# Kernel optimization log

Hardware: AMD Instinct MI355X
Metric: run time of the kernel (lower is better)

Reference implementation:

```python
import jax, jax.numpy as jnp
import numpy as np

N_NODES = 50000
D_IN = 256
D_OUT = 128
N_POS = 1600000   # positive edges used for GCN aggregation
N_PRED = 500000   # edges to score


def setup_inputs() -> dict:
    key = jax.random.key(0)
    ks = jax.random.split(key, 6)
    x = jax.random.normal(ks[0], (N_NODES, D_IN), dtype=jnp.float32)
    pos_edge_index = jax.random.randint(ks[1], (2, N_POS), 0, N_NODES)
    edge_index = jax.random.randint(ks[2], (2, N_PRED), 0, N_NODES)
    # init_linear: Linear(d_in, d_in); stored as (in, out) so fwd is x @ W1 + b1
    W1 = jax.random.normal(ks[3], (D_IN, D_IN), dtype=jnp.float32) / np.sqrt(D_IN).astype(np.float32)
    b1 = jnp.zeros((D_IN,), dtype=jnp.float32)
    # GCNConv weight (in, out) and bias
    Wc = jax.random.normal(ks[4], (D_IN, D_OUT), dtype=jnp.float32) / np.sqrt(D_IN).astype(np.float32)
    bc = jnp.zeros((D_OUT,), dtype=jnp.float32)
    return dict(x=x, edge_index=edge_index, pos_edge_index=pos_edge_index,
                W1=W1, b1=b1, Wc=Wc, bc=bc)


def reference(x, edge_index, pos_edge_index, W1, b1, Wc, bc):
    n = x.shape[0]
    # init_linear
    h = x @ W1 + b1                                  # [N, D_IN]
    # GCNConv: linear transform first, then normalized scatter-add aggregation
    h = h @ Wc                                       # [N, D_OUT]
    # add self-loops (PyG GCNConv default add_self_loops=True, edge_weight=1)
    loops = jnp.arange(n, dtype=pos_edge_index.dtype)
    row = jnp.concatenate([pos_edge_index[0], loops])  # source
    col = jnp.concatenate([pos_edge_index[1], loops])  # target (aggregation)
    # symmetric normalization: deg over target, norm = d^-1/2[row]*d^-1/2[col]
    deg = jax.ops.segment_sum(jnp.ones_like(col, dtype=h.dtype), col, num_segments=n)
    dinv = jnp.where(deg > 0, jax.lax.rsqrt(deg), 0.0)
    norm = dinv[row] * dinv[col]                     # [E+N]
    msgs = h[row] * norm[:, None]                    # gather + scale
    out = jax.ops.segment_sum(msgs, col, num_segments=n) + bc  # scatter-add + bias
    # edge dot-product scoring
    logits = (out[edge_index[0]] * out[edge_index[1]]).sum(axis=-1)  # [N_PRED]
    return logits
```

## Files before the change

kernel.cpp:

```cpp
#include <hip/hip_runtime.h>

#define N_NODES 50000
#define D_IN 256
#define D_OUT 128
#define N_POS 1600000
#define N_PRED 500000

#define G_BUCKETS 782
#define GPAD 1024
#define SB 640
#define CHUNK 2500
#define CAP 4096
#define GEMM_BLOCKS 782
#define QPRED 125000

#define NT 4
#define TSZ 12500
#define NPB 32
#define AGGB 1563

typedef __attribute__((ext_vector_type(8))) short short8;
typedef __attribute__((ext_vector_type(4))) float f32x4;

__device__ __forceinline__ unsigned short f2bf(float f) {
    unsigned int u = __float_as_uint(f);
    u += 0x7FFFu + ((u >> 16) & 1u);
    return (unsigned short)(u >> 16);
}
__device__ __forceinline__ unsigned int pk2(float a, float b) {
    unsigned int ua = __float_as_uint(a), ub = __float_as_uint(b);
    ua += 0x7FFFu + ((ua >> 16) & 1u);
    ub += 0x7FFFu + ((ub >> 16) & 1u);
    return (ua >> 16) | (ub & 0xFFFF0000u);
}
__device__ __forceinline__ float bflo(unsigned int u) { return __uint_as_float(u << 16); }
__device__ __forceinline__ float bfhi(unsigned int u) { return __uint_as_float(u & 0xFFFF0000u); }

__device__ __forceinline__ float dot8(uint4 ua, uint4 ub) {
    return bflo(ua.x) * bflo(ub.x) + bfhi(ua.x) * bfhi(ub.x)
         + bflo(ua.y) * bflo(ub.y) + bfhi(ua.y) * bfhi(ub.y)
         + bflo(ua.z) * bflo(ub.z) + bfhi(ua.z) * bfhi(ub.z)
         + bflo(ua.w) * bflo(ub.w) + bfhi(ua.w) * bfhi(ub.w);
}

__global__ void fuse_weights_k(const float* __restrict__ W1, const float* __restrict__ Wc,
                               const float* __restrict__ b1,
                               unsigned short* __restrict__ Bp, float* __restrict__ bf) {
    int gid = blockIdx.x * blockDim.x + threadIdx.x;
    int k = gid >> 7;
    int n = gid & 127;
    float acc = 0.f;
    #pragma unroll 4
    for (int kk = 0; kk < D_IN; ++kk)
        acc += W1[k * D_IN + kk] * Wc[kk * D_OUT + n];
    int ks = k >> 5, q = (k >> 3) & 3, jj = k & 7;
    int nt = n >> 4, nl = n & 15;
    int lane = q * 16 + nl;
    Bp[(((long)(ks * 8 + nt)) * 64 + lane) * 8 + jj] = f2bf(acc);
    if (gid < D_OUT) {
        float accb = 0.f;
        for (int kk = 0; kk < D_IN; ++kk)
            accb += b1[kk] * Wc[kk * D_OUT + gid];
        bf[gid] = accb;
    }
}

__global__ __launch_bounds__(256) void scatter_gemm_k(const int* __restrict__ row,
                                                      const int* __restrict__ col,
                                                      unsigned int* __restrict__ seg,
                                                      unsigned int* __restrict__ ebs,
                                                      const float* __restrict__ x,
                                                      const uint4* __restrict__ Bp,
                                                      const float* __restrict__ bf,
                                                      unsigned short* __restrict__ hsb) {
    __shared__ __align__(16) char smem[23424];
    if (blockIdx.x < SB) {
        int* hist  = (int*)smem;
        int* lofs  = hist + GPAD;
        int* fill2 = lofs + GPAD;
        int* part  = fill2 + GPAD;
        unsigned int* stag = (unsigned int*)(part + 256);
        int t = threadIdx.x;
        int b = blockIdx.x;
        for (int i = t; i < GPAD; i += 256) { hist[i] = 0; fill2[i] = 0; }
        __syncthreads();
        int e0 = b * CHUNK;
        for (int i = t; i < CHUNK; i += 256)
            atomicAdd(&hist[col[e0 + i] >> 6], 1);
        __syncthreads();
        int h[4], p4 = 0;
        #pragma unroll
        for (int i = 0; i < 4; ++i) { h[i] = hist[4 * t + i]; p4 += h[i]; }
        part[t] = p4;
        __syncthreads();
        for (int d = 1; d < 256; d <<= 1) {
            int add = (t >= d) ? part[t - d] : 0;
            __syncthreads();
            part[t] += add;
            __syncthreads();
        }
        int ex = part[t] - p4;
        #pragma unroll
        for (int i = 0; i < 4; ++i) { lofs[4 * t + i] = ex; ex += h[i]; }
        __syncthreads();
        for (int g = t; g < G_BUCKETS; g += 256)
            seg[(long)g * SB + b] = (unsigned int)lofs[g] | ((unsigned int)hist[g] << 16);
        for (int i = t; i < CHUNK; i += 256) {
            int c = col[e0 + i];
            int g = c >> 6;
            unsigned int u = (unsigned int)row[e0 + i] | ((unsigned int)(c & 63) << 16);
            int lp = atomicAdd(&fill2[g], 1);
            stag[lofs[g] + lp] = u;
        }
        __syncthreads();
        for (int i = t; i < CHUNK; i += 256)
            ebs[(long)b * CHUNK + i] = stag[i];
    } else {
        const int gb   = blockIdx.x - SB;
        const int wave = threadIdx.x >> 6;
        const int lane = threadIdx.x & 63;
        const int q    = lane >> 4;
        const int ml   = lane & 15;
        const int m0   = gb * 64 + wave * 16;

        f32x4 acc[8];
        #pragma unroll
        for (int t = 0; t < 8; ++t) acc[t] = (f32x4){0.f, 0.f, 0.f, 0.f};

        long arow = m0 + ml; if (arow > N_NODES - 1) arow = N_NODES - 1;
        const float* xrow = x + arow * D_IN + q * 8;

        #pragma unroll
        for (int ks = 0; ks < 8; ++ks) {
            float4 xa = *(const float4*)(xrow + ks * 32);
            float4 xb = *(const float4*)(xrow + ks * 32 + 4);
            union { short8 s; unsigned int u[4]; } af;
            af.u[0] = pk2(xa.x, xa.y);
            af.u[1] = pk2(xa.z, xa.w);
            af.u[2] = pk2(xb.x, xb.y);
            af.u[3] = pk2(xb.z, xb.w);
            #pragma unroll
            for (int nt = 0; nt < 8; ++nt) {
                union { uint4 v; short8 s; } bu;
                bu.v = Bp[(long)(ks * 8 + nt) * 64 + lane];
                acc[nt] = __builtin_amdgcn_mfma_f32_16x16x32_bf16(af.s, bu.s, acc[nt], 0, 0, 0);
            }
        }

        unsigned short* o = (unsigned short*)smem + wave * 2048;
        #pragma unroll
        for (int nt = 0; nt < 8; ++nt) {
            float bn = bf[nt * 16 + ml];
            #pragma unroll
            for (int r = 0; r < 4; ++r) {
                float val = acc[nt][r] + bn;
                o[(q * 4 + r) * 128 + nt * 16 + ml] = f2bf(val);
            }
        }
        __syncthreads();
        #pragma unroll
        for (int i = 0; i < 4; ++i) {
            int fb = i * 1024 + lane * 16;
            int v = m0 + (fb >> 8);
            if (v < N_NODES) {
                uint4 val = *(const uint4*)((const char*)o + fb);
                *(uint4*)((char*)hsb + (long)v * 256 + (fb & 255)) = val;
            }
        }
    }
}

__global__ __launch_bounds__(256) void csr_build_k(const unsigned int* __restrict__ seg,
                                                   const unsigned int* __restrict__ ebs,
                                                   unsigned short* __restrict__ csr,
                                                   int* __restrict__ offs5,
                                                   float* __restrict__ dinv,
                                                   uint4* __restrict__ hsb4) {
    __shared__ unsigned int stag[CAP];
    __shared__ unsigned short stag2[CAP];
    __shared__ int hist[256], lofs[256], fill[256], part[256];
    __shared__ float dloc[64];
    __shared__ int scnt;
    int t = threadIdx.x;
    int g = blockIdx.x;
    int s = g * CAP;
    hist[t] = 0; fill[t] = 0;
    const unsigned int* sg = seg + (long)g * SB;
    unsigned int w0 = sg[t];
    unsigned int w1 = sg[t + 256];
    unsigned int w2 = (t + 512 < SB) ? sg[t + 512] : 0u;
    int c0 = w0 >> 16, c1 = w1 >> 16, c2 = w2 >> 16;
    int lsum = c0 + c1 + c2;
    part[t] = lsum;
    __syncthreads();
    for (int d = 1; d < 256; d <<= 1) {
        int add = (t >= d) ? part[t - d] : 0;
        __syncthreads();
        part[t] += add;
        __syncthreads();
    }
    if (t == 255) scnt = part[255];
    int p = part[t] - lsum;
    {
        const unsigned int* e0p = ebs + (long)t * CHUNK + (w0 & 0xFFFFu);
        for (int k = 0; k < c0; ++k) stag[p + k] = e0p[k];
        p += c0;
        const unsigned int* e1p = ebs + (long)(t + 256) * CHUNK + (w1 & 0xFFFFu);
        for (int k = 0; k < c1; ++k) stag[p + k] = e1p[k];
        p += c1;
        const unsigned int* e2p = ebs + (long)(t + 512) * CHUNK + (w2 & 0xFFFFu);
        for (int k = 0; k < c2; ++k) stag[p + k] = e2p[k];
    }
    __syncthreads();
    int cnt = scnt;
    for (int i = t; i < cnt; i += 256) {
        unsigned int u = stag[i];
        int r = u & 0xFFFF;
        int tile = (r >= TSZ) + (r >= 2 * TSZ) + (r >= 3 * TSZ);
        atomicAdd(&hist[((u >> 16) & 63) * NT + tile], 1);
    }
    __syncthreads();
    int hv = hist[t];
    part[t] = hv;
    __syncthreads();
    for (int d = 1; d < 256; d <<= 1) {
        int add = (t >= d) ? part[t - d] : 0;
        __syncthreads();
        part[t] += add;
        __syncthreads();
    }
    lofs[t] = part[t] - hv;
    __syncthreads();
    if (t < 64) {
        int v = g * 64 + t;
        int b4 = t * NT;
        int cc0 = hist[b4], cc1 = hist[b4 + 1], cc2 = hist[b4 + 2], cc3 = hist[b4 + 3];
        float dl = rsqrtf((float)(cc0 + cc1 + cc2 + cc3) + 1.0f);
        dloc[t] = dl;
        if (v < N_NODES) {
            int o0 = s + lofs[b4];
            offs5[v * 5 + 0] = o0;
            offs5[v * 5 + 1] = o0 + cc0;
            offs5[v * 5 + 2] = o0 + cc0 + cc1;
            offs5[v * 5 + 3] = o0 + cc0 + cc1 + cc2;
            offs5[v * 5 + 4] = o0 + cc0 + cc1 + cc2 + cc3;
            dinv[v] = dl;
        }
    }
    for (int i = t; i < cnt; i += 256) {
        unsigned int u = stag[i];
        int r = u & 0xFFFF;
        int tile = (r >= TSZ) + (r >= 2 * TSZ) + (r >= 3 * TSZ);
        int key = ((u >> 16) & 63) * NT + tile;
        int lp = atomicAdd(&fill[key], 1);
        stag2[lofs[key] + lp] = (unsigned short)r;
    }
    __syncthreads();
    for (int i = t; i < cnt; i += 256)
        csr[s + i] = stag2[i];
    const int vb = g * 64;
    for (int i = t; i < 64 * 16; i += 256) {
        int n = i >> 4;
        int v = vb + n;
        if (v < N_NODES) {
            float d = dloc[n];
            long idx = (long)v * 16 + (i & 15);
            uint4 u = hsb4[idx];
            uint4 o;
            o.x = pk2(d * bflo(u.x), d * bfhi(u.x));
            o.y = pk2(d * bflo(u.y), d * bfhi(u.y));
            o.z = pk2(d * bflo(u.z), d * bfhi(u.z));
            o.w = pk2(d * bflo(u.w), d * bfhi(u.w));
            hsb4[idx] = o;
        }
    }
}

__global__ __launch_bounds__(256, 8) void aggregate_csr_k(const int* __restrict__ offs5,
                                                          const unsigned short* __restrict__ csr,
                                                          const uint4* __restrict__ hs4,
                                                          const float* __restrict__ dinv,
                                                          const float* __restrict__ bc,
                                                          uint4* __restrict__ feat4) {
    int tid = threadIdx.x;
    int li  = tid & 15;
    int g16 = tid >> 4;
    int v0 = blockIdx.x * NPB + g16 * 2;
    int v1 = v0 + 1;
    bool ok0 = v0 < N_NODES, ok1 = v1 < N_NODES;

    float a0[8] = {0.f, 0.f, 0.f, 0.f, 0.f, 0.f, 0.f, 0.f};
    float a1[8] = {0.f, 0.f, 0.f, 0.f, 0.f, 0.f, 0.f, 0.f};

    #pragma unroll 1
    for (int tt = 0; tt < NT; ++tt) {
        if (ok0) {
            int i  = offs5[v0 * 5 + tt];
            int s1 = offs5[v0 * 5 + tt + 1];
            for (; i + 3 < s1; i += 4) {
                int r0 = csr[i], r1 = csr[i + 1], r2 = csr[i + 2], r3 = csr[i + 3];
                uint4 u0 = hs4[r0 * 16 + li];
                uint4 u1 = hs4[r1 * 16 + li];
                uint4 u2 = hs4[r2 * 16 + li];
                uint4 u3 = hs4[r3 * 16 + li];
                a0[0] += (bflo(u0.x) + bflo(u1.x)) + (bflo(u2.x) + bflo(u3.x));
                a0[1] += (bfhi(u0.x) + bfhi(u1.x)) + (bfhi(u2.x) + bfhi(u3.x));
                a0[2] += (bflo(u0.y) + bflo(u1.y)) + (bflo(u2.y) + bflo(u3.y));
                a0[3] += (bfhi(u0.y) + bfhi(u1.y)) + (bfhi(u2.y) + bfhi(u3.y));
                a0[4] += (bflo(u0.z) + bflo(u1.z)) + (bflo(u2.z) + bflo(u3.z));
                a0[5] += (bfhi(u0.z) + bfhi(u1.z)) + (bfhi(u2.z) + bfhi(u3.z));
                a0[6] += (bflo(u0.w) + bflo(u1.w)) + (bflo(u2.w) + bflo(u3.w));
                a0[7] += (bfhi(u0.w) + bfhi(u1.w)) + (bfhi(u2.w) + bfhi(u3.w));
            }
            for (; i < s1; ++i) {
                int r = csr[i];
                uint4 u = hs4[r * 16 + li];
                a0[0] += bflo(u.x); a0[1] += bfhi(u.x);
                a0[2] += bflo(u.y); a0[3] += bfhi(u.y);
                a0[4] += bflo(u.z); a0[5] += bfhi(u.z);
                a0[6] += bflo(u.w); a0[7] += bfhi(u.w);
            }
        }
        if (ok1) {
            int i  = offs5[v1 * 5 + tt];
            int s1 = offs5[v1 * 5 + tt + 1];
            for (; i + 3 < s1; i += 4) {
                int r0 = csr[i], r1 = csr[i + 1], r2 = csr[i + 2], r3 = csr[i + 3];
                uint4 u0 = hs4[r0 * 16 + li];
                uint4 u1 = hs4[r1 * 16 + li];
                uint4 u2 = hs4[r2 * 16 + li];
                uint4 u3 = hs4[r3 * 16 + li];
                a1[0] += (bflo(u0.x) + bflo(u1.x)) + (bflo(u2.x) + bflo(u3.x));
                a1[1] += (bfhi(u0.x) + bfhi(u1.x)) + (bfhi(u2.x) + bfhi(u3.x));
                a1[2] += (bflo(u0.y) + bflo(u1.y)) + (bflo(u2.y) + bflo(u3.y));
                a1[3] += (bfhi(u0.y) + bfhi(u1.y)) + (bfhi(u2.y) + bfhi(u3.y));
                a1[4] += (bflo(u0.z) + bflo(u1.z)) + (bflo(u2.z) + bflo(u3.z));
                a1[5] += (bfhi(u0.z) + bfhi(u1.z)) + (bfhi(u2.z) + bfhi(u3.z));
                a1[6] += (bflo(u0.w) + bflo(u1.w)) + (bflo(u2.w) + bflo(u3.w));
                a1[7] += (bfhi(u0.w) + bfhi(u1.w)) + (bfhi(u2.w) + bfhi(u3.w));
            }
            for (; i < s1; ++i) {
                int r = csr[i];
                uint4 u = hs4[r * 16 + li];
                a1[0] += bflo(u.x); a1[1] += bfhi(u.x);
                a1[2] += bflo(u.y); a1[3] += bfhi(u.y);
                a1[4] += bflo(u.z); a1[5] += bfhi(u.z);
                a1[6] += bflo(u.w); a1[7] += bfhi(u.w);
            }
        }
    }
    float4 b0 = *(const float4*)(bc + li * 8);
    float4 b1 = *(const float4*)(bc + li * 8 + 4);
    if (ok0) {
        uint4 su = hs4[(long)v0 * 16 + li];
        float dv = dinv[v0];
        float f0 = dv * (a0[0] + bflo(su.x)) + b0.x;
        float f1 = dv * (a0[1] + bfhi(su.x)) + b0.y;
        float f2 = dv * (a0[2] + bflo(su.y)) + b0.z;
        float f3 = dv * (a0[3] + bfhi(su.y)) + b0.w;
        float f4 = dv * (a0[4] + bflo(su.z)) + b1.x;
        float f5 = dv * (a0[5] + bfhi(su.z)) + b1.y;
        float f6 = dv * (a0[6] + bflo(su.w)) + b1.z;
        float f7 = dv * (a0[7] + bfhi(su.w)) + b1.w;
        uint4 o;
        o.x = pk2(f0, f1); o.y = pk2(f2, f3); o.z = pk2(f4, f5); o.w = pk2(f6, f7);
        feat4[(long)v0 * 16 + li] = o;
    }
    if (ok1) {
        uint4 su = hs4[(long)v1 * 16 + li];
        float dv = dinv[v1];
        float f0 = dv * (a1[0] + bflo(su.x)) + b0.x;
        float f1 = dv * (a1[1] + bfhi(su.x)) + b0.y;
        float f2 = dv * (a1[2] + bflo(su.y)) + b0.z;
        float f3 = dv * (a1[3] + bfhi(su.y)) + b0.w;
        float f4 = dv * (a1[4] + bflo(su.z)) + b1.x;
        float f5 = dv * (a1[5] + bfhi(su.z)) + b1.y;
        float f6 = dv * (a1[6] + bflo(su.w)) + b1.z;
        float f7 = dv * (a1[7] + bfhi(su.w)) + b1.w;
        uint4 o;
        o.x = pk2(f0, f1); o.y = pk2(f2, f3); o.z = pk2(f4, f5); o.w = pk2(f6, f7);
        feat4[(long)v1 * 16 + li] = o;
    }
}

__global__ void score_k(const int* __restrict__ src, const int* __restrict__ dst,
                        const uint4* __restrict__ feat4, float* __restrict__ out) {
    int gid = blockIdx.x * blockDim.x + threadIdx.x;
    int e = gid >> 4;
    int c = gid & 15;
    if (e >= QPRED) return;
    int e0 = e, e1 = e + QPRED, e2 = e + 2 * QPRED, e3 = e + 3 * QPRED;
    int a0 = src[e0], b0 = dst[e0];
    int a1 = src[e1], b1 = dst[e1];
    int a2 = src[e2], b2 = dst[e2];
    int a3 = src[e3], b3 = dst[e3];
    uint4 ua0 = feat4[(long)a0 * 16 + c];
    uint4 ub0 = feat4[(long)b0 * 16 + c];
    uint4 ua1 = feat4[(long)a1 * 16 + c];
    uint4 ub1 = feat4[(long)b1 * 16 + c];
    uint4 ua2 = feat4[(long)a2 * 16 + c];
    uint4 ub2 = feat4[(long)b2 * 16 + c];
    uint4 ua3 = feat4[(long)a3 * 16 + c];
    uint4 ub3 = feat4[(long)b3 * 16 + c];
    float p0 = dot8(ua0, ub0);
    float p1 = dot8(ua1, ub1);
    float p2 = dot8(ua2, ub2);
    float p3 = dot8(ua3, ub3);
    #pragma unroll
    for (int m = 8; m; m >>= 1) {
        p0 += __shfl_xor(p0, m, 16);
        p1 += __shfl_xor(p1, m, 16);
        p2 += __shfl_xor(p2, m, 16);
        p3 += __shfl_xor(p3, m, 16);
    }
    if (c == 0) {
        out[e0] = p0;
        out[e1] = p1;
        out[e2] = p2;
        out[e3] = p3;
    }
}

extern "C" void kernel_launch(void* const* d_in, const int* in_sizes, int n_in,
                              void* d_out, int out_size, void* d_ws, size_t ws_size,
                              hipStream_t stream) {
    const float* x   = (const float*)d_in[0];
    const int*   ei  = (const int*)  d_in[1];
    const int*   pe  = (const int*)  d_in[2];
    const float* W1  = (const float*)d_in[3];
    const float* b1  = (const float*)d_in[4];
    const float* Wc  = (const float*)d_in[5];
    const float* bc  = (const float*)d_in[6];
    float* out = (float*)d_out;

    const int* pe_row = pe;
    const int* pe_col = pe + N_POS;
    const int* ei_src = ei;
    const int* ei_dst = ei + N_PRED;

    char* w = (char*)d_ws;
    unsigned short* Bp = (unsigned short*)w;  w += 32768 * 2;
    float* bf    = (float*)w;                 w += 128 * 4;
    float* dinv  = (float*)w;                 w += 50000 * 4;
    int*   offs5 = (int*)w;                   w += 50000 * 5 * 4;
    unsigned int* seg = (unsigned int*)w;     w += (long)G_BUCKETS * SB * 4;
    unsigned int* ebs = (unsigned int*)w;     w += (long)SB * CHUNK * 4;
    unsigned short* csr = (unsigned short*)w; w += (long)G_BUCKETS * CAP * 2;
    unsigned short* hsb   = (unsigned short*)w;  w += (long)N_NODES * D_OUT * 2;
    unsigned short* featb = (unsigned short*)w;

    fuse_weights_k<<<128, 256, 0, stream>>>(W1, Wc, b1, Bp, bf);

    scatter_gemm_k<<<SB + GEMM_BLOCKS, 256, 0, stream>>>(pe_row, pe_col, seg, ebs,
                                                         x, (const uint4*)Bp, bf, hsb);

    csr_build_k   <<<G_BUCKETS, 256, 0, stream>>>(seg, ebs, csr, offs5, dinv,
                                                  (uint4*)hsb);

    aggregate_csr_k<<<AGGB, 256, 0, stream>>>(offs5, csr, (const uint4*)hsb,
                                              dinv, bc, (uint4*)featb);

    score_k       <<<(QPRED * 16 + 255) / 256, 256, 0, stream>>>(
                      ei_src, ei_dst, (const uint4*)featb, out);
}
```

Measured before the change: 243.1 us.

## Overlap weight fusion with edge scatter and widen CSR aggregation per thread group

The weight-fusion work now runs as extra blocks inside the edge-scatter kernel, so it overlaps with the scatter, and the node-feature GEMM becomes its own kernel launched afterwards. The launch count stays the same, and the GEMM no longer shares a launch with the scatter blocks. The aggregation kernel now handles three nodes per 16-lane group instead of two, adds an 8-way unrolled gather loop for more memory-level parallelism, and relaxes launch bounds to 4 blocks per SM. The cost is higher register pressure, lower occupancy and fewer aggregation blocks.

```diff
diff --git a/kernel.cpp b/kernel.cpp
--- a/kernel.cpp
+++ b/kernel.cpp
@@ -16,8 +16,9 @@
 
 #define NT 4
 #define TSZ 12500
-#define NPB 32
-#define AGGB 1563
+#define NPG 3
+#define NPB 48
+#define AGGB 1042
 
 typedef __attribute__((ext_vector_type(8))) short short8;
 typedef __attribute__((ext_vector_type(4))) float f32x4;
@@ -43,36 +44,15 @@
          + bflo(ua.w) * bflo(ub.w) + bfhi(ua.w) * bfhi(ub.w);
 }
 
-__global__ void fuse_weights_k(const float* __restrict__ W1, const float* __restrict__ Wc,
-                               const float* __restrict__ b1,
-                               unsigned short* __restrict__ Bp, float* __restrict__ bf) {
-    int gid = blockIdx.x * blockDim.x + threadIdx.x;
-    int k = gid >> 7;
-    int n = gid & 127;
-    float acc = 0.f;
-    #pragma unroll 4
-    for (int kk = 0; kk < D_IN; ++kk)
-        acc += W1[k * D_IN + kk] * Wc[kk * D_OUT + n];
-    int ks = k >> 5, q = (k >> 3) & 3, jj = k & 7;
-    int nt = n >> 4, nl = n & 15;
-    int lane = q * 16 + nl;
-    Bp[(((long)(ks * 8 + nt)) * 64 + lane) * 8 + jj] = f2bf(acc);
-    if (gid < D_OUT) {
-        float accb = 0.f;
-        for (int kk = 0; kk < D_IN; ++kk)
-            accb += b1[kk] * Wc[kk * D_OUT + gid];
-        bf[gid] = accb;
-    }
-}
-
-__global__ __launch_bounds__(256) void scatter_gemm_k(const int* __restrict__ row,
+__global__ __launch_bounds__(256) void scatter_fuse_k(const int* __restrict__ row,
                                                       const int* __restrict__ col,
                                                       unsigned int* __restrict__ seg,
                                                       unsigned int* __restrict__ ebs,
-                                                      const float* __restrict__ x,
-                                                      const uint4* __restrict__ Bp,
-                                                      const float* __restrict__ bf,
-                                                      unsigned short* __restrict__ hsb) {
+                                                      const float* __restrict__ W1,
+                                                      const float* __restrict__ Wc,
+                                                      const float* __restrict__ b1,
+                                                      unsigned short* __restrict__ Bp,
+                                                      float* __restrict__ bf) {
     __shared__ __align__(16) char smem[23424];
     if (blockIdx.x < SB) {
         int* hist  = (int*)smem;
@@ -116,56 +96,79 @@
         for (int i = t; i < CHUNK; i += 256)
             ebs[(long)b * CHUNK + i] = stag[i];
     } else {
-        const int gb   = blockIdx.x - SB;
-        const int wave = threadIdx.x >> 6;
-        const int lane = threadIdx.x & 63;
-        const int q    = lane >> 4;
-        const int ml   = lane & 15;
-        const int m0   = gb * 64 + wave * 16;
-
-        f32x4 acc[8];
-        #pragma unroll
-        for (int t = 0; t < 8; ++t) acc[t] = (f32x4){0.f, 0.f, 0.f, 0.f};
-
-        long arow = m0 + ml; if (arow > N_NODES - 1) arow = N_NODES - 1;
-        const float* xrow = x + arow * D_IN + q * 8;
-
-        #pragma unroll
-        for (int ks = 0; ks < 8; ++ks) {
-            float4 xa = *(const float4*)(xrow + ks * 32);
-            float4 xb = *(const float4*)(xrow + ks * 32 + 4);
-            union { short8 s; unsigned int u[4]; } af;
-            af.u[0] = pk2(xa.x, xa.y);
-            af.u[1] = pk2(xa.z, xa.w);
-            af.u[2] = pk2(xb.x, xb.y);
-            af.u[3] = pk2(xb.z, xb.w);
-            #pragma unroll
-            for (int nt = 0; nt < 8; ++nt) {
-                union { uint4 v; short8 s; } bu;
-                bu.v = Bp[(long)(ks * 8 + nt) * 64 + lane];
-                acc[nt] = __builtin_amdgcn_mfma_f32_16x16x32_bf16(af.s, bu.s, acc[nt], 0, 0, 0);
-            }
-        }
-
-        unsigned short* o = (unsigned short*)smem + wave * 2048;
+        int gid = (blockIdx.x - SB) * 256 + threadIdx.x;
+        int k = gid >> 7;
+        int n = gid & 127;
+        float acc = 0.f;
+        #pragma unroll 4
+        for (int kk = 0; kk < D_IN; ++kk)
+            acc += W1[k * D_IN + kk] * Wc[kk * D_OUT + n];
+        int ks = k >> 5, q = (k >> 3) & 3, jj = k & 7;
+        int nt = n >> 4, nl = n & 15;
+        int lane = q * 16 + nl;
+        Bp[(((long)(ks * 8 + nt)) * 64 + lane) * 8 + jj] = f2bf(acc);
+        if (gid < D_OUT) {
+            float accb = 0.f;
+            for (int kk = 0; kk < D_IN; ++kk)
+                accb += b1[kk] * Wc[kk * D_OUT + gid];
+            bf[gid] = accb;
+        }
+    }
+}
+
+__global__ __launch_bounds__(256) void gemm_k(const float* __restrict__ x,
+                                              const uint4* __restrict__ Bp,
+                                              const float* __restrict__ bf,
+                                              unsigned short* __restrict__ hsb) {
+    __shared__ __align__(16) char smem[16384];
+    const int wave = threadIdx.x >> 6;
+    const int lane = threadIdx.x & 63;
+    const int q    = lane >> 4;
+    const int ml   = lane & 15;
+    const int m0   = blockIdx.x * 64 + wave * 16;
+
+    f32x4 acc[8];
+    #pragma unroll
+    for (int t = 0; t < 8; ++t) acc[t] = (f32x4){0.f, 0.f, 0.f, 0.f};
+
+    long arow = m0 + ml; if (arow > N_NODES - 1) arow = N_NODES - 1;
+    const float* xrow = x + arow * D_IN + q * 8;
+
+    #pragma unroll
+    for (int ks = 0; ks < 8; ++ks) {
+        float4 xa = *(const float4*)(xrow + ks * 32);
+        float4 xb = *(const float4*)(xrow + ks * 32 + 4);
+        union { short8 s; unsigned int u[4]; } af;
+        af.u[0] = pk2(xa.x, xa.y);
+        af.u[1] = pk2(xa.z, xa.w);
+        af.u[2] = pk2(xb.x, xb.y);
+        af.u[3] = pk2(xb.z, xb.w);
         #pragma unroll
         for (int nt = 0; nt < 8; ++nt) {
-            float bn = bf[nt * 16 + ml];
-            #pragma unroll
-            for (int r = 0; r < 4; ++r) {
-                float val = acc[nt][r] + bn;
-                o[(q * 4 + r) * 128 + nt * 16 + ml] = f2bf(val);
-            }
-        }
-        __syncthreads();
-        #pragma unroll
-        for (int i = 0; i < 4; ++i) {
-            int fb = i * 1024 + lane * 16;
-            int v = m0 + (fb >> 8);
-            if (v < N_NODES) {
-                uint4 val = *(const uint4*)((const char*)o + fb);
-                *(uint4*)((char*)hsb + (long)v * 256 + (fb & 255)) = val;
-            }
+            union { uint4 v; short8 s; } bu;
+            bu.v = Bp[(long)(ks * 8 + nt) * 64 + lane];
+            acc[nt] = __builtin_amdgcn_mfma_f32_16x16x32_bf16(af.s, bu.s, acc[nt], 0, 0, 0);
+        }
+    }
+
+    unsigned short* o = (unsigned short*)smem + wave * 2048;
+    #pragma unroll
+    for (int nt = 0; nt < 8; ++nt) {
+        float bn = bf[nt * 16 + ml];
+        #pragma unroll
+        for (int r = 0; r < 4; ++r) {
+            float val = acc[nt][r] + bn;
+            o[(q * 4 + r) * 128 + nt * 16 + ml] = f2bf(val);
+        }
+    }
+    __syncthreads();
+    #pragma unroll
+    for (int i = 0; i < 4; ++i) {
+        int fb = i * 1024 + lane * 16;
+        int v = m0 + (fb >> 8);
+        if (v < N_NODES) {
+            uint4 val = *(const uint4*)((const char*)o + fb);
+            *(uint4*)((char*)hsb + (long)v * 256 + (fb & 255)) = val;
         }
     }
 }
@@ -276,7 +279,7 @@
     }
 }
 
-__global__ __launch_bounds__(256, 8) void aggregate_csr_k(const int* __restrict__ offs5,
+__global__ __launch_bounds__(256, 4) void aggregate_csr_k(const int* __restrict__ offs5,
                                                           const unsigned short* __restrict__ csr,
                                                           const uint4* __restrict__ hs4,
                                                           const float* __restrict__ dinv,
@@ -285,101 +288,94 @@
     int tid = threadIdx.x;
     int li  = tid & 15;
     int g16 = tid >> 4;
-    int v0 = blockIdx.x * NPB + g16 * 2;
-    int v1 = v0 + 1;
-    bool ok0 = v0 < N_NODES, ok1 = v1 < N_NODES;
-
-    float a0[8] = {0.f, 0.f, 0.f, 0.f, 0.f, 0.f, 0.f, 0.f};
-    float a1[8] = {0.f, 0.f, 0.f, 0.f, 0.f, 0.f, 0.f, 0.f};
+    int vb  = blockIdx.x * NPB + g16 * NPG;
+
+    float a[NPG][8];
+    #pragma unroll
+    for (int n = 0; n < NPG; ++n)
+        #pragma unroll
+        for (int j = 0; j < 8; ++j) a[n][j] = 0.f;
 
     #pragma unroll 1
     for (int tt = 0; tt < NT; ++tt) {
-        if (ok0) {
-            int i  = offs5[v0 * 5 + tt];
-            int s1 = offs5[v0 * 5 + tt + 1];
+        #pragma unroll
+        for (int n = 0; n < NPG; ++n) {
+            int v = vb + n;
+            if (v >= N_NODES) continue;
+            int i  = offs5[v * 5 + tt];
+            int s1 = offs5[v * 5 + tt + 1];
+            for (; i + 7 < s1; i += 8) {
+                int r0 = csr[i],     r1 = csr[i + 1], r2 = csr[i + 2], r3 = csr[i + 3];
+                int r4 = csr[i + 4], r5 = csr[i + 5], r6 = csr[i + 6], r7 = csr[i + 7];
+                uint4 u0 = hs4[r0 * 16 + li];
+                uint4 u1 = hs4[r1 * 16 + li];
+                uint4 u2 = hs4[r2 * 16 + li];
+                uint4 u3 = hs4[r3 * 16 + li];
+                uint4 u4 = hs4[r4 * 16 + li];
+                uint4 u5 = hs4[r5 * 16 + li];
+                uint4 u6 = hs4[r6 * 16 + li];
+                uint4 u7 = hs4[r7 * 16 + li];
+                a[n][0] += ((bflo(u0.x) + bflo(u1.x)) + (bflo(u2.x) + bflo(u3.x)))
+                         + ((bflo(u4.x) + bflo(u5.x)) + (bflo(u6.x) + bflo(u7.x)));
+                a[n][1] += ((bfhi(u0.x) + bfhi(u1.x)) + (bfhi(u2.x) + bfhi(u3.x)))
+                         + ((bfhi(u4.x) + bfhi(u5.x)) + (bfhi(u6.x) + bfhi(u7.x)));
+                a[n][2] += ((bflo(u0.y) + bflo(u1.y)) + (bflo(u2.y) + bflo(u3.y)))
+                         + ((bflo(u4.y) + bflo(u5.y)) + (bflo(u6.y) + bflo(u7.y)));
+                a[n][3] += ((bfhi(u0.y) + bfhi(u1.y)) + (bfhi(u2.y) + bfhi(u3.y)))
+                         + ((bfhi(u4.y) + bfhi(u5.y)) + (bfhi(u6.y) + bfhi(u7.y)));
+                a[n][4] += ((bflo(u0.z) + bflo(u1.z)) + (bflo(u2.z) + bflo(u3.z)))
+                         + ((bflo(u4.z) + bflo(u5.z)) + (bflo(u6.z) + bflo(u7.z)));
+                a[n][5] += ((bfhi(u0.z) + bfhi(u1.z)) + (bfhi(u2.z) + bfhi(u3.z)))
+                         + ((bfhi(u4.z) + bfhi(u5.z)) + (bfhi(u6.z) + bfhi(u7.z)));
+                a[n][6] += ((bflo(u0.w) + bflo(u1.w)) + (bflo(u2.w) + bflo(u3.w)))
+                         + ((bflo(u4.w) + bflo(u5.w)) + (bflo(u6.w) + bflo(u7.w)));
+                a[n][7] += ((bfhi(u0.w) + bfhi(u1.w)) + (bfhi(u2.w) + bfhi(u3.w)))
+                         + ((bfhi(u4.w) + bfhi(u5.w)) + (bfhi(u6.w) + bfhi(u7.w)));
+            }
             for (; i + 3 < s1; i += 4) {
                 int r0 = csr[i], r1 = csr[i + 1], r2 = csr[i + 2], r3 = csr[i + 3];
                 uint4 u0 = hs4[r0 * 16 + li];
                 uint4 u1 = hs4[r1 * 16 + li];
                 uint4 u2 = hs4[r2 * 16 + li];
                 uint4 u3 = hs4[r3 * 16 + li];
-                a0[0] += (bflo(u0.x) + bflo(u1.x)) + (bflo(u2.x) + bflo(u3.x));
-                a0[1] += (bfhi(u0.x) + bfhi(u1.x)) + (bfhi(u2.x) + bfhi(u3.x));
-                a0[2] += (bflo(u0.y) + bflo(u1.y)) + (bflo(u2.y) + bflo(u3.y));
-                a0[3] += (bfhi(u0.y) + bfhi(u1.y)) + (bfhi(u2.y) + bfhi(u3.y));
-                a0[4] += (bflo(u0.z) + bflo(u1.z)) + (bflo(u2.z) + bflo(u3.z));
-                a0[5] += (bfhi(u0.z) + bfhi(u1.z)) + (bfhi(u2.z) + bfhi(u3.z));
-                a0[6] += (bflo(u0.w) + bflo(u1.w)) + (bflo(u2.w) + bflo(u3.w));
-                a0[7] += (bfhi(u0.w) + bfhi(u1.w)) + (bfhi(u2.w) + bfhi(u3.w));
+                a[n][0] += (bflo(u0.x) + bflo(u1.x)) + (bflo(u2.x) + bflo(u3.x));
+                a[n][1] += (bfhi(u0.x) + bfhi(u1.x)) + (bfhi(u2.x) + bfhi(u3.x));
+                a[n][2] += (bflo(u0.y) + bflo(u1.y)) + (bflo(u2.y) + bflo(u3.y));
+                a[n][3] += (bfhi(u0.y) + bfhi(u1.y)) + (bfhi(u2.y) + bfhi(u3.y));
+                a[n][4] += (bflo(u0.z) + bflo(u1.z)) + (bflo(u2.z) + bflo(u3.z));
+                a[n][5] += (bfhi(u0.z) + bfhi(u1.z)) + (bfhi(u2.z) + bfhi(u3.z));
+                a[n][6] += (bflo(u0.w) + bflo(u1.w)) + (bflo(u2.w) + bflo(u3.w));
+                a[n][7] += (bfhi(u0.w) + bfhi(u1.w)) + (bfhi(u2.w) + bfhi(u3.w));
             }
             for (; i < s1; ++i) {
                 int r = csr[i];
                 uint4 u = hs4[r * 16 + li];
-                a0[0] += bflo(u.x); a0[1] += bfhi(u.x);
-                a0[2] += bflo(u.y); a0[3] += bfhi(u.y);
-                a0[4] += bflo(u.z); a0[5] += bfhi(u.z);
-                a0[6] += bflo(u.w); a0[7] += bfhi(u.w);
-            }
-        }
-        if (ok1) {
-            int i  = offs5[v1 * 5 + tt];
-            int s1 = offs5[v1 * 5 + tt + 1];
-            for (; i + 3 < s1; i += 4) {
-                int r0 = csr[i], r1 = csr[i + 1], r2 = csr[i + 2], r3 = csr[i + 3];
-                uint4 u0 = hs4[r0 * 16 + li];
-                uint4 u1 = hs4[r1 * 16 + li];
-                uint4 u2 = hs4[r2 * 16 + li];
-                uint4 u3 = hs4[r3 * 16 + li];
-                a1[0] += (bflo(u0.x) + bflo(u1.x)) + (bflo(u2.x) + bflo(u3.x));
-                a1[1] += (bfhi(u0.x) + bfhi(u1.x)) + (bfhi(u2.x) + bfhi(u3.x));
-                a1[2] += (bflo(u0.y) + bflo(u1.y)) + (bflo(u2.y) + bflo(u3.y));
-                a1[3] += (bfhi(u0.y) + bfhi(u1.y)) + (bfhi(u2.y) + bfhi(u3.y));
-                a1[4] += (bflo(u0.z) + bflo(u1.z)) + (bflo(u2.z) + bflo(u3.z));
-                a1[5] += (bfhi(u0.z) + bfhi(u1.z)) + (bfhi(u2.z) + bfhi(u3.z));
-                a1[6] += (bflo(u0.w) + bflo(u1.w)) + (bflo(u2.w) + bflo(u3.w));
-                a1[7] += (bfhi(u0.w) + bfhi(u1.w)) + (bfhi(u2.w) + bfhi(u3.w));
-            }
-            for (; i < s1; ++i) {
-                int r = csr[i];
-                uint4 u = hs4[r * 16 + li];
-                a1[0] += bflo(u.x); a1[1] += bfhi(u.x);
-                a1[2] += bflo(u.y); a1[3] += bfhi(u.y);
-                a1[4] += bflo(u.z); a1[5] += bfhi(u.z);
-                a1[6] += bflo(u.w); a1[7] += bfhi(u.w);
+                a[n][0] += bflo(u.x); a[n][1] += bfhi(u.x);
+                a[n][2] += bflo(u.y); a[n][3] += bfhi(u.y);
+                a[n][4] += bflo(u.z); a[n][5] += bfhi(u.z);
+                a[n][6] += bflo(u.w); a[n][7] += bfhi(u.w);
             }
         }
     }
     float4 b0 = *(const float4*)(bc + li * 8);
     float4 b1 = *(const float4*)(bc + li * 8 + 4);
-    if (ok0) {
-        uint4 su = hs4[(long)v0 * 16 + li];
-        float dv = dinv[v0];
-        float f0 = dv * (a0[0] + bflo(su.x)) + b0.x;
-        float f1 = dv * (a0[1] + bfhi(su.x)) + b0.y;
-        float f2 = dv * (a0[2] + bflo(su.y)) + b0.z;
-        float f3 = dv * (a0[3] + bfhi(su.y)) + b0.w;
-        float f4 = dv * (a0[4] + bflo(su.z)) + b1.x;
-        float f5 = dv * (a0[5] + bfhi(su.z)) + b1.y;
-        float f6 = dv * (a0[6] + bflo(su.w)) + b1.z;
-        float f7 = dv * (a0[7] + bfhi(su.w)) + b1.w;
+    #pragma unroll
+    for (int n = 0; n < NPG; ++n) {
+        int v = vb + n;
+        if (v >= N_NODES) continue;
+        uint4 su = hs4[(long)v * 16 + li];
+        float dv = dinv[v];
+        float f0 = dv * (a[n][0] + bflo(su.x)) + b0.x;
+        float f1 = dv * (a[n][1] + bfhi(su.x)) + b0.y;
+        float f2 = dv * (a[n][2] + bflo(su.y)) + b0.z;
+        float f3 = dv * (a[n][3] + bfhi(su.y)) + b0.w;
+        float f4 = dv * (a[n][4] + bflo(su.z)) + b1.x;
+        float f5 = dv * (a[n][5] + bfhi(su.z)) + b1.y;
+        float f6 = dv * (a[n][6] + bflo(su.w)) + b1.z;
+        float f7 = dv * (a[n][7] + bfhi(su.w)) + b1.w;
         uint4 o;
         o.x = pk2(f0, f1); o.y = pk2(f2, f3); o.z = pk2(f4, f5); o.w = pk2(f6, f7);
-        feat4[(long)v0 * 16 + li] = o;
-    }
-    if (ok1) {
-        uint4 su = hs4[(long)v1 * 16 + li];
-        float dv = dinv[v1];
-        float f0 = dv * (a1[0] + bflo(su.x)) + b0.x;
-        float f1 = dv * (a1[1] + bfhi(su.x)) + b0.y;
-        float f2 = dv * (a1[2] + bflo(su.y)) + b0.z;
-        float f3 = dv * (a1[3] + bfhi(su.y)) + b0.w;
-        float f4 = dv * (a1[4] + bflo(su.z)) + b1.x;
-        float f5 = dv * (a1[5] + bfhi(su.z)) + b1.y;
-        float f6 = dv * (a1[6] + bflo(su.w)) + b1.z;
-        float f7 = dv * (a1[7] + bfhi(su.w)) + b1.w;
-        uint4 o;
-        o.x = pk2(f0, f1); o.y = pk2(f2, f3); o.z = pk2(f4, f5); o.w = pk2(f6, f7);
-        feat4[(long)v1 * 16 + li] = o;
+        feat4[(long)v * 16 + li] = o;
     }
 }
 
@@ -449,10 +445,10 @@
     unsigned short* hsb   = (unsigned short*)w;  w += (long)N_NODES * D_OUT * 2;
     unsigned short* featb = (unsigned short*)w;
 
-    fuse_weights_k<<<128, 256, 0, stream>>>(W1, Wc, b1, Bp, bf);
-
-    scatter_gemm_k<<<SB + GEMM_BLOCKS, 256, 0, stream>>>(pe_row, pe_col, seg, ebs,
-                                                         x, (const uint4*)Bp, bf, hsb);
+    scatter_fuse_k<<<SB + 128, 256, 0, stream>>>(pe_row, pe_col, seg, ebs,
+                                                 W1, Wc, b1, Bp, bf);
+
+    gemm_k        <<<GEMM_BLOCKS, 256, 0, stream>>>(x, (const uint4*)Bp, bf, hsb);
 
     csr_build_k   <<<G_BUCKETS, 256, 0, stream>>>(seg, ebs, csr, offs5, dinv,
                                                   (uint4*)hsb);
```

After: 277.9 us. 14.3% more time.
